# Kernel optimization log

Measured on AMD Instinct MI355X. Metric: run time of the kernel, lower is better.

Reference implementation:

```python
import jax, jax.numpy as jnp
import numpy as np

B, S, IN, OUT = 8, 2048, 1024, 4096
QMAX = 255.0  # 2**8 - 1 levels for 8-bit


def _quantize(x):
    """Per-tensor affine int8 quantization, matching Int8Linear.quantize."""
    x_max = x.max()
    x_min = x.min()
    scale = (x_max - x_min) / QMAX
    zero_point = jnp.round((x_max * -128.0 - x_min * 127.0) / (x_max - x_min))
    # torch does .to(torch.int8): wrapping cast; round has zero grad, int cast detaches
    x_q = jax.lax.stop_gradient((jnp.round(x / scale) + zero_point).astype(jnp.int8))
    return x_q, scale, zero_point


def setup_inputs() -> dict:
    key = jax.random.key(0)
    kx, kw, kb = jax.random.split(key, 3)
    x = jax.random.normal(kx, (B, S, IN), dtype=jnp.float32)
    w = jax.random.normal(kw, (OUT, IN), dtype=jnp.float32) * 0.02  # nn.Linear-ish init scale
    w_q, w_scale, w_zp = _quantize(w)  # done once at module init in torch
    bias = jax.random.normal(kb, (OUT,), dtype=jnp.float32) * 0.01
    return {
        "x": x,
        "w_q": w_q.astype(jnp.int32),  # stored int8 values, carried as int32
        "w_scale": w_scale,
        "w_zp": w_zp,
        "bias": bias,
    }


def reference(x, w_q, w_scale, w_zp, bias):
    # quantize activation per call (per-tensor affine)
    x_q, x_scale, x_zp = _quantize(x)
    # torch: matmul(x_q.to(int32) - x_zero_point, weight.T.to(int32) - zero_point)
    # zero points are FLOAT tensors, so the subtraction promotes to float32 and the
    # GEMM runs in float32 on centered integer-valued operands.
    xc = x_q.astype(jnp.float32) - x_zp            # [B, S, IN]
    wc = w_q.astype(jnp.float32) - w_zp            # [OUT, IN]
    acc = jnp.einsum('bsi,oi->bso', xc, wc)        # [B, S, OUT]
    return acc * (x_scale * w_scale) + bias
```

## Files before the change

### kernel.cpp

```cpp
#include <hip/hip_runtime.h>
#include <stdint.h>

#define M_ROWS 16384
#define N_COLS 4096
#define K_DIM  1024
#define NT     (K_DIM / 64)

typedef __bf16 bf16x8 __attribute__((ext_vector_type(8)));
typedef float  f32x4  __attribute__((ext_vector_type(4)));

__device__ __forceinline__ void gload_lds16(const void* g, void* l) {
    __builtin_amdgcn_global_load_lds(
        (const __attribute__((address_space(1))) unsigned int*)g,
        (__attribute__((address_space(3))) unsigned int*)l, 16, 0, 0);
}

#define SBAR() do { __builtin_amdgcn_sched_barrier(0); \
                    __builtin_amdgcn_s_barrier();      \
                    __builtin_amdgcn_sched_barrier(0); } while (0)

__device__ __forceinline__ unsigned short f32_to_bf16_exact(float f) {
    return (unsigned short)(__builtin_bit_cast(unsigned int, f) >> 16);
}

__global__ void k_minmax(const float4* __restrict__ x,
                         float* __restrict__ pmax, float* __restrict__ pmin) {
    const int n4 = (M_ROWS * K_DIM) / 4;
    float mx = -3.402823466e38f, mn = 3.402823466e38f;
    for (int i = blockIdx.x * blockDim.x + threadIdx.x; i < n4;
         i += gridDim.x * blockDim.x) {
        float4 v = x[i];
        mx = fmaxf(mx, fmaxf(fmaxf(v.x, v.y), fmaxf(v.z, v.w)));
        mn = fminf(mn, fminf(fminf(v.x, v.y), fminf(v.z, v.w)));
    }
#pragma unroll
    for (int off = 32; off > 0; off >>= 1) {
        mx = fmaxf(mx, __shfl_xor(mx, off));
        mn = fminf(mn, __shfl_xor(mn, off));
    }
    __shared__ float smx[4], smn[4];
    const int wave = threadIdx.x >> 6, lane = threadIdx.x & 63;
    if (lane == 0) { smx[wave] = mx; smn[wave] = mn; }
    __syncthreads();
    if (threadIdx.x == 0) {
        mx = fmaxf(fmaxf(smx[0], smx[1]), fmaxf(smx[2], smx[3]));
        mn = fminf(fminf(smn[0], smn[1]), fminf(smn[2], smn[3]));
        pmax[blockIdx.x] = mx;
        pmin[blockIdx.x] = mn;
    }
}

__global__ void k_scalars(const float* __restrict__ pmax, const float* __restrict__ pmin,
                          const float* __restrict__ w_scale, float* __restrict__ scal) {
    float mx = -3.402823466e38f, mn = 3.402823466e38f;
    for (int i = threadIdx.x; i < 2048; i += 256) {
        mx = fmaxf(mx, pmax[i]);
        mn = fminf(mn, pmin[i]);
    }
#pragma unroll
    for (int off = 32; off > 0; off >>= 1) {
        mx = fmaxf(mx, __shfl_xor(mx, off));
        mn = fminf(mn, __shfl_xor(mn, off));
    }
    __shared__ float smx[4], smn[4];
    const int wave = threadIdx.x >> 6, lane = threadIdx.x & 63;
    if (lane == 0) { smx[wave] = mx; smn[wave] = mn; }
    __syncthreads();
    if (threadIdx.x == 0) {
        mx = fmaxf(fmaxf(smx[0], smx[1]), fmaxf(smx[2], smx[3]));
        mn = fminf(fminf(smn[0], smn[1]), fminf(smn[2], smn[3]));
        const float scale = (mx - mn) / 255.0f;
        const float zp = rintf((mx * -128.0f - mn * 127.0f) / (mx - mn));
        scal[0] = scale;
        scal[1] = zp;
        scal[2] = scale * w_scale[0];
    }
}

__global__ void k_quant(const float4* __restrict__ x, const float* __restrict__ scal,
                        ushort4* __restrict__ xc) {
    const float scale = scal[0], zp = scal[1];
    const int n4 = (M_ROWS * K_DIM) / 4;
    for (int i = blockIdx.x * blockDim.x + threadIdx.x; i < n4;
         i += gridDim.x * blockDim.x) {
        float4 v = x[i];
        ushort4 o;
        int q0 = (int)(rintf(v.x / scale) + zp);
        int q1 = (int)(rintf(v.y / scale) + zp);
        int q2 = (int)(rintf(v.z / scale) + zp);
        int q3 = (int)(rintf(v.w / scale) + zp);
        o.x = f32_to_bf16_exact((float)(signed char)q0 - zp);
        o.y = f32_to_bf16_exact((float)(signed char)q1 - zp);
        o.z = f32_to_bf16_exact((float)(signed char)q2 - zp);
        o.w = f32_to_bf16_exact((float)(signed char)q3 - zp);
        xc[i] = o;
    }
}

__global__ void k_prepw(const int4* __restrict__ wq, const float* __restrict__ wzp,
                        ushort4* __restrict__ wc) {
    const float zp = wzp[0];
    const int n4 = (N_COLS * K_DIM) / 4;
    for (int i = blockIdx.x * blockDim.x + threadIdx.x; i < n4;
         i += gridDim.x * blockDim.x) {
        int4 v = wq[i];
        ushort4 o;
        o.x = f32_to_bf16_exact((float)v.x - zp);
        o.y = f32_to_bf16_exact((float)v.y - zp);
        o.z = f32_to_bf16_exact((float)v.z - zp);
        o.w = f32_to_bf16_exact((float)v.w - zp);
        wc[i] = o;
    }
}

__global__ __launch_bounds__(512, 2)
void k_gemm(const unsigned short* __restrict__ A,
            const unsigned short* __restrict__ B,
            const float* __restrict__ scal,
            const float* __restrict__ bias,
            float* __restrict__ C) {
    __shared__ char lds[131072];

    const int tid  = threadIdx.x;
    const int wave = tid >> 6, lane = tid & 63;
    const int wm = wave >> 2, wn = wave & 3;
    const int fr = lane & 15, kg = lane >> 4;

    const int wg  = blockIdx.x;
    const int swz = ((wg & 7) << 7) | (wg >> 3);
    const int bm  = swz >> 4;
    const int bn  = swz & 15;

    const int scol = ((tid & 7) ^ ((tid >> 3) & 7)) << 4;
    const char* gA = (const char*)A + (size_t)(bm * 256 + (tid >> 3)) * (K_DIM * 2) + scol;
    const char* gB = (const char*)B + (size_t)(bn * 256 + (tid >> 3)) * (K_DIM * 2) + scol;

#define STAGE_A(tt, h, b) do {                                          \
        const char* g_ = gA + (size_t)(tt) * 128 + (size_t)(h) * 262144; \
        char* l_ = lds + (b) * 32768 + (h) * 16384 + wave * 1024;        \
        gload_lds16(g_, l_);                                             \
        gload_lds16(g_ + 131072, l_ + 8192);                             \
    } while (0)
#define STAGE_B(tt, h, b) do {                                          \
        const char* g_ = gB + (size_t)(tt) * 128 + (size_t)(h) * 262144; \
        char* l_ = lds + 65536 + (b) * 32768 + (h) * 16384 + wave * 1024; \
        gload_lds16(g_, l_);                                             \
        gload_lds16(g_ + 131072, l_ + 8192);                             \
    } while (0)

    const int kx0 = ((kg * 16) ^ ((fr & 7) << 4));
    const int kx1 = ((64 + kg * 16) ^ ((fr & 7) << 4));
    const int arow = (wm * 128 + fr) * 128;
    const int brow = (wn * 64 + fr) * 128;

    f32x4 acc[8][4] = {};
    bf16x8 bf[4][2];

    STAGE_A(0, 0, 0); STAGE_A(0, 1, 0);
    STAGE_B(0, 0, 0); STAGE_B(0, 1, 0);
    STAGE_B(1, 0, 1); STAGE_B(1, 1, 1);
    asm volatile("s_waitcnt vmcnt(4)" ::: "memory");
    SBAR();

    for (int t = 0; t < NT; ++t) {
        const int b = t & 1;
        const char* Ab = lds + b * 32768;
        const char* Bb = lds + 65536 + b * 32768;
#pragma unroll
        for (int q = 0; q < 4; ++q) {
            bf16x8 af[2][2];
            if (q == 0) {
#pragma unroll
                for (int j = 0; j < 4; ++j) {
                    bf[j][0] = *(const bf16x8*)(Bb + brow + j * 2048 + kx0);
                    bf[j][1] = *(const bf16x8*)(Bb + brow + j * 2048 + kx1);
                }
            }
#pragma unroll
            for (int i2 = 0; i2 < 2; ++i2) {
                const int i = 2 * q + i2;
                af[i2][0] = *(const bf16x8*)(Ab + arow + i * 2048 + kx0);
                af[i2][1] = *(const bf16x8*)(Ab + arow + i * 2048 + kx1);
            }
            if (q == 0)      { if (t + 1 < NT) STAGE_A(t + 1, 0, b ^ 1); }
            else if (q == 1) { if (t + 1 < NT) STAGE_A(t + 1, 1, b ^ 1); }
            else if (q == 2) { if (t + 2 < NT) STAGE_B(t + 2, 0, b); }
            else {
                if (t + 2 < NT) {
                    STAGE_B(t + 2, 1, b);
                    asm volatile("s_waitcnt vmcnt(4)" ::: "memory");
                } else {
                    asm volatile("s_waitcnt vmcnt(0)" ::: "memory");
                }
            }
            SBAR();
            __builtin_amdgcn_s_setprio(1);
#pragma unroll
            for (int kk = 0; kk < 2; ++kk)
#pragma unroll
                for (int i2 = 0; i2 < 2; ++i2)
#pragma unroll
                    for (int j = 0; j < 4; ++j)
                        acc[2 * q + i2][j] = __builtin_amdgcn_mfma_f32_16x16x32_bf16(
                            af[i2][kk], bf[j][kk], acc[2 * q + i2][j], 0, 0, 0);
            __builtin_amdgcn_s_setprio(0);
            SBAR();
        }
    }

    const float alpha = scal[2];
    const int gc_base = bn * 256 + wn * 64;
    const int gr_base = bm * 256 + wm * 128;
#pragma unroll
    for (int j = 0; j < 4; ++j) {
        const int gc = gc_base + j * 16 + fr;
        const float bv = bias[gc];
#pragma unroll
        for (int i = 0; i < 8; ++i) {
            const int gr0 = gr_base + i * 16 + kg * 4;
#pragma unroll
            for (int r = 0; r < 4; ++r)
                C[(size_t)(gr0 + r) * N_COLS + gc] = acc[i][j][r] * alpha + bv;
        }
    }
#undef STAGE_A
#undef STAGE_B
}

extern "C" void kernel_launch(void* const* d_in, const int* in_sizes, int n_in,
                              void* d_out, int out_size, void* d_ws, size_t ws_size,
                              hipStream_t stream) {
    const float* x    = (const float*)d_in[0];
    const int*   wq   = (const int*)d_in[1];
    const float* wsc  = (const float*)d_in[2];
    const float* wzp  = (const float*)d_in[3];
    const float* bias = (const float*)d_in[4];
    float* out = (float*)d_out;

    char* ws = (char*)d_ws;
    unsigned short* xc = (unsigned short*)(ws);
    unsigned short* wc = (unsigned short*)(ws + 33554432);
    float* pmax = (float*)(ws + 41943040);
    float* pmin = (float*)(ws + 41951232);
    float* scal = (float*)(ws + 41959424);

    k_prepw  <<<2048, 256, 0, stream>>>((const int4*)wq, wzp, (ushort4*)wc);
    k_minmax <<<2048, 256, 0, stream>>>((const float4*)x, pmax, pmin);
    k_scalars<<<1,    256, 0, stream>>>(pmax, pmin, wsc, scal);
    k_quant  <<<2048, 256, 0, stream>>>((const float4*)x, scal, (ushort4*)xc);
    k_gemm   <<<1024, 512, 0, stream>>>(xc, wc, scal, bias, out);
}
```

Baseline: 469.9 us.

## Switch GEMM to int8 MFMA with zero-point row/column sum corrections

Measured after the change: 407.4 us. 13.3% less time.

```diff
diff --git a/kernel.cpp b/kernel.cpp
--- a/kernel.cpp
+++ b/kernel.cpp
@@ -4,10 +4,10 @@
 #define M_ROWS 16384
 #define N_COLS 4096
 #define K_DIM  1024
-#define NT     (K_DIM / 64)
-
-typedef __bf16 bf16x8 __attribute__((ext_vector_type(8)));
-typedef float  f32x4  __attribute__((ext_vector_type(4)));
+#define NT     (K_DIM / 128)
+
+typedef int   i32x4 __attribute__((ext_vector_type(4)));
+typedef float f32x4 __attribute__((ext_vector_type(4)));
 
 __device__ __forceinline__ void gload_lds16(const void* g, void* l) {
     __builtin_amdgcn_global_load_lds(
@@ -18,10 +18,6 @@
 #define SBAR() do { __builtin_amdgcn_sched_barrier(0); \
                     __builtin_amdgcn_s_barrier();      \
                     __builtin_amdgcn_sched_barrier(0); } while (0)
-
-__device__ __forceinline__ unsigned short f32_to_bf16_exact(float f) {
-    return (unsigned short)(__builtin_bit_cast(unsigned int, f) >> 16);
-}
 
 __global__ void k_minmax(const float4* __restrict__ x,
                          float* __restrict__ pmax, float* __restrict__ pmin) {
@@ -77,47 +73,68 @@
     }
 }
 
-__global__ void k_quant(const float4* __restrict__ x, const float* __restrict__ scal,
-                        ushort4* __restrict__ xc) {
-    const float scale = scal[0], zp = scal[1];
-    const int n4 = (M_ROWS * K_DIM) / 4;
-    for (int i = blockIdx.x * blockDim.x + threadIdx.x; i < n4;
-         i += gridDim.x * blockDim.x) {
-        float4 v = x[i];
-        ushort4 o;
-        int q0 = (int)(rintf(v.x / scale) + zp);
-        int q1 = (int)(rintf(v.y / scale) + zp);
-        int q2 = (int)(rintf(v.z / scale) + zp);
-        int q3 = (int)(rintf(v.w / scale) + zp);
-        o.x = f32_to_bf16_exact((float)(signed char)q0 - zp);
-        o.y = f32_to_bf16_exact((float)(signed char)q1 - zp);
-        o.z = f32_to_bf16_exact((float)(signed char)q2 - zp);
-        o.w = f32_to_bf16_exact((float)(signed char)q3 - zp);
-        xc[i] = o;
-    }
-}
-
-__global__ void k_prepw(const int4* __restrict__ wq, const float* __restrict__ wzp,
-                        ushort4* __restrict__ wc) {
-    const float zp = wzp[0];
-    const int n4 = (N_COLS * K_DIM) / 4;
-    for (int i = blockIdx.x * blockDim.x + threadIdx.x; i < n4;
-         i += gridDim.x * blockDim.x) {
-        int4 v = wq[i];
-        ushort4 o;
-        o.x = f32_to_bf16_exact((float)v.x - zp);
-        o.y = f32_to_bf16_exact((float)v.y - zp);
-        o.z = f32_to_bf16_exact((float)v.z - zp);
-        o.w = f32_to_bf16_exact((float)v.w - zp);
-        wc[i] = o;
+__global__ void k_quant(const float* __restrict__ x, const float* __restrict__ scal,
+                        const float* __restrict__ wzp,
+                        int4* __restrict__ xc8, float* __restrict__ cm) {
+    const float scale = scal[0], zx = scal[1], zw = wzp[0];
+    const int lane = threadIdx.x & 63;
+    const int gw = (blockIdx.x * blockDim.x + threadIdx.x) >> 6;
+    const int nw = (gridDim.x * blockDim.x) >> 6;
+    for (int row = gw; row < M_ROWS; row += nw) {
+        const float4* xr = (const float4*)(x + (size_t)row * K_DIM + lane * 16);
+        union { signed char c[16]; int4 v; } u;
+        int s = 0;
+#pragma unroll
+        for (int e = 0; e < 4; ++e) {
+            float4 v = xr[e];
+            signed char c0 = (signed char)(int)(rintf(v.x / scale) + zx);
+            signed char c1 = (signed char)(int)(rintf(v.y / scale) + zx);
+            signed char c2 = (signed char)(int)(rintf(v.z / scale) + zx);
+            signed char c3 = (signed char)(int)(rintf(v.w / scale) + zx);
+            u.c[e * 4 + 0] = c0; u.c[e * 4 + 1] = c1;
+            u.c[e * 4 + 2] = c2; u.c[e * 4 + 3] = c3;
+            s += (int)c0 + (int)c1 + (int)c2 + (int)c3;
+        }
+        xc8[row * 64 + lane] = u.v;
+#pragma unroll
+        for (int off = 32; off > 0; off >>= 1) s += __shfl_xor(s, off);
+        if (lane == 0) cm[row] = zw * (1024.0f * zx - (float)s);
+    }
+}
+
+__global__ void k_prepw(const int* __restrict__ wq, const float* __restrict__ scal,
+                        int4* __restrict__ wc8, float* __restrict__ cn) {
+    const float zx = scal[1];
+    const int lane = threadIdx.x & 63;
+    const int gw = (blockIdx.x * blockDim.x + threadIdx.x) >> 6;
+    const int nw = (gridDim.x * blockDim.x) >> 6;
+    for (int row = gw; row < N_COLS; row += nw) {
+        const int4* wr = (const int4*)(wq + (size_t)row * K_DIM + lane * 16);
+        union { signed char c[16]; int4 v; } u;
+        int s = 0;
+#pragma unroll
+        for (int e = 0; e < 4; ++e) {
+            int4 v = wr[e];
+            u.c[e * 4 + 0] = (signed char)v.x;
+            u.c[e * 4 + 1] = (signed char)v.y;
+            u.c[e * 4 + 2] = (signed char)v.z;
+            u.c[e * 4 + 3] = (signed char)v.w;
+            s += v.x + v.y + v.z + v.w;
+        }
+        wc8[row * 64 + lane] = u.v;
+#pragma unroll
+        for (int off = 32; off > 0; off >>= 1) s += __shfl_xor(s, off);
+        if (lane == 0) cn[row] = -zx * (float)s;
     }
 }
 
 __global__ __launch_bounds__(512, 2)
-void k_gemm(const unsigned short* __restrict__ A,
-            const unsigned short* __restrict__ B,
+void k_gemm(const signed char* __restrict__ A,
+            const signed char* __restrict__ B,
             const float* __restrict__ scal,
             const float* __restrict__ bias,
+            const float* __restrict__ cm,
+            const float* __restrict__ cn,
             float* __restrict__ C) {
     __shared__ char lds[131072];
 
@@ -132,20 +149,20 @@
     const int bn  = swz & 15;
 
     const int scol = ((tid & 7) ^ ((tid >> 3) & 7)) << 4;
-    const char* gA = (const char*)A + (size_t)(bm * 256 + (tid >> 3)) * (K_DIM * 2) + scol;
-    const char* gB = (const char*)B + (size_t)(bn * 256 + (tid >> 3)) * (K_DIM * 2) + scol;
-
-#define STAGE_A(tt, h, b) do {                                          \
-        const char* g_ = gA + (size_t)(tt) * 128 + (size_t)(h) * 262144; \
+    const char* gA = (const char*)A + (size_t)(bm * 256 + (tid >> 3)) * K_DIM + scol;
+    const char* gB = (const char*)B + (size_t)(bn * 256 + (tid >> 3)) * K_DIM + scol;
+
+#define STAGE_A(tt, h, b) do {                                           \
+        const char* g_ = gA + (size_t)(tt) * 128 + (size_t)(h) * 131072; \
         char* l_ = lds + (b) * 32768 + (h) * 16384 + wave * 1024;        \
         gload_lds16(g_, l_);                                             \
-        gload_lds16(g_ + 131072, l_ + 8192);                             \
+        gload_lds16(g_ + 65536, l_ + 8192);                              \
     } while (0)
-#define STAGE_B(tt, h, b) do {                                          \
-        const char* g_ = gB + (size_t)(tt) * 128 + (size_t)(h) * 262144; \
+#define STAGE_B(tt, h, b) do {                                           \
+        const char* g_ = gB + (size_t)(tt) * 128 + (size_t)(h) * 131072; \
         char* l_ = lds + 65536 + (b) * 32768 + (h) * 16384 + wave * 1024; \
         gload_lds16(g_, l_);                                             \
-        gload_lds16(g_ + 131072, l_ + 8192);                             \
+        gload_lds16(g_ + 65536, l_ + 8192);                              \
     } while (0)
 
     const int kx0 = ((kg * 16) ^ ((fr & 7) << 4));
@@ -153,8 +170,8 @@
     const int arow = (wm * 128 + fr) * 128;
     const int brow = (wn * 64 + fr) * 128;
 
-    f32x4 acc[8][4] = {};
-    bf16x8 bf[4][2];
+    i32x4 acc[8][4] = {};
+    i32x4 bf[4][2];
 
     STAGE_A(0, 0, 0); STAGE_A(0, 1, 0);
     STAGE_B(0, 0, 0); STAGE_B(0, 1, 0);
@@ -168,19 +185,19 @@
         const char* Bb = lds + 65536 + b * 32768;
 #pragma unroll
         for (int q = 0; q < 4; ++q) {
-            bf16x8 af[2][2];
+            i32x4 af[2][2];
             if (q == 0) {
 #pragma unroll
                 for (int j = 0; j < 4; ++j) {
-                    bf[j][0] = *(const bf16x8*)(Bb + brow + j * 2048 + kx0);
-                    bf[j][1] = *(const bf16x8*)(Bb + brow + j * 2048 + kx1);
+                    bf[j][0] = *(const i32x4*)(Bb + brow + j * 2048 + kx0);
+                    bf[j][1] = *(const i32x4*)(Bb + brow + j * 2048 + kx1);
                 }
             }
 #pragma unroll
             for (int i2 = 0; i2 < 2; ++i2) {
                 const int i = 2 * q + i2;
-                af[i2][0] = *(const bf16x8*)(Ab + arow + i * 2048 + kx0);
-                af[i2][1] = *(const bf16x8*)(Ab + arow + i * 2048 + kx1);
+                af[i2][0] = *(const i32x4*)(Ab + arow + i * 2048 + kx0);
+                af[i2][1] = *(const i32x4*)(Ab + arow + i * 2048 + kx1);
             }
             if (q == 0)      { if (t + 1 < NT) STAGE_A(t + 1, 0, b ^ 1); }
             else if (q == 1) { if (t + 1 < NT) STAGE_A(t + 1, 1, b ^ 1); }
@@ -201,7 +218,7 @@
                 for (int i2 = 0; i2 < 2; ++i2)
 #pragma unroll
                     for (int j = 0; j < 4; ++j)
-                        acc[2 * q + i2][j] = __builtin_amdgcn_mfma_f32_16x16x32_bf16(
+                        acc[2 * q + i2][j] = __builtin_amdgcn_mfma_i32_16x16x64_i8(
                             af[i2][kk], bf[j][kk], acc[2 * q + i2][j], 0, 0, 0);
             __builtin_amdgcn_s_setprio(0);
             SBAR();
@@ -211,16 +228,24 @@
     const float alpha = scal[2];
     const int gc_base = bn * 256 + wn * 64;
     const int gr_base = bm * 256 + wm * 128;
+    float bb[4], cc[4];
 #pragma unroll
     for (int j = 0; j < 4; ++j) {
         const int gc = gc_base + j * 16 + fr;
-        const float bv = bias[gc];
-#pragma unroll
-        for (int i = 0; i < 8; ++i) {
-            const int gr0 = gr_base + i * 16 + kg * 4;
-#pragma unroll
-            for (int r = 0; r < 4; ++r)
-                C[(size_t)(gr0 + r) * N_COLS + gc] = acc[i][j][r] * alpha + bv;
+        bb[j] = bias[gc];
+        cc[j] = cn[gc];
+    }
+#pragma unroll
+    for (int i = 0; i < 8; ++i) {
+        const int gr0 = gr_base + i * 16 + kg * 4;
+        const float4 cmv = *(const float4*)(cm + gr0);
+#pragma unroll
+        for (int j = 0; j < 4; ++j) {
+            const int gc = gc_base + j * 16 + fr;
+            C[(size_t)(gr0 + 0) * N_COLS + gc] = ((float)acc[i][j][0] + cmv.x + cc[j]) * alpha + bb[j];
+            C[(size_t)(gr0 + 1) * N_COLS + gc] = ((float)acc[i][j][1] + cmv.y + cc[j]) * alpha + bb[j];
+            C[(size_t)(gr0 + 2) * N_COLS + gc] = ((float)acc[i][j][2] + cmv.z + cc[j]) * alpha + bb[j];
+            C[(size_t)(gr0 + 3) * N_COLS + gc] = ((float)acc[i][j][3] + cmv.w + cc[j]) * alpha + bb[j];
         }
     }
 #undef STAGE_A
@@ -238,15 +263,18 @@
     float* out = (float*)d_out;
 
     char* ws = (char*)d_ws;
-    unsigned short* xc = (unsigned short*)(ws);
-    unsigned short* wc = (unsigned short*)(ws + 33554432);
-    float* pmax = (float*)(ws + 41943040);
-    float* pmin = (float*)(ws + 41951232);
-    float* scal = (float*)(ws + 41959424);
-
-    k_prepw  <<<2048, 256, 0, stream>>>((const int4*)wq, wzp, (ushort4*)wc);
+    int4*  xc8  = (int4*)(ws);
+    int4*  wc8  = (int4*)(ws + 16777216);
+    float* cm   = (float*)(ws + 20971520);
+    float* cn   = (float*)(ws + 21037056);
+    float* pmax = (float*)(ws + 21053440);
+    float* pmin = (float*)(ws + 21061632);
+    float* scal = (float*)(ws + 21069824);
+
     k_minmax <<<2048, 256, 0, stream>>>((const float4*)x, pmax, pmin);
     k_scalars<<<1,    256, 0, stream>>>(pmax, pmin, wsc, scal);
-    k_quant  <<<2048, 256, 0, stream>>>((const float4*)x, scal, (ushort4*)xc);
-    k_gemm   <<<1024, 512, 0, stream>>>(xc, wc, scal, bias, out);
-}
+    k_prepw  <<<1024, 256, 0, stream>>>(wq, scal, wc8, cn);
+    k_quant  <<<2048, 256, 0, stream>>>(x, scal, wzp, xc8, cm);
+    k_gemm   <<<1024, 512, 0, stream>>>((const signed char*)xc8, (const signed char*)wc8,
+                                        scal, bias, cm, cn, out);
+}
```
